# Kernel tuning notes

Measured on AMD Instinct MI355X. Metric: run time of the kernel, lower is better.

The kernel has to match this reference:

```python
import jax, jax.numpy as jnp
import numpy as np

DIM = 2048        # config.dim
HID = 1408        # config.moe_inter_dim
E = 16            # config.n_routed_experts
TOPK = 4          # config.n_activated_experts
SHARED = 2816     # n_shared_experts * moe_inter_dim
B, S = 1, 2048
ROUTE_SCALE = 1.0


def setup_inputs() -> dict:
    key = jax.random.key(0)
    ks = jax.random.split(key, 8)
    def w(k, shape, fan_in):
        return jax.random.normal(k, shape, jnp.float32) * (1.0 / np.sqrt(fan_in))
    return {
        "x": jax.random.normal(ks[0], (B, S, DIM), jnp.float32),
        "gate_w": w(ks[1], (E, DIM), DIM),
        "w1": w(ks[2], (E, HID, DIM), DIM),   # per-expert nn.Linear(dim, hid).weight
        "w2": w(ks[3], (E, DIM, HID), HID),   # per-expert nn.Linear(hid, dim).weight
        "w3": w(ks[4], (E, HID, DIM), DIM),
        "sw1": w(ks[5], (SHARED, DIM), DIM),  # shared MLP weights
        "sw2": w(ks[6], (DIM, SHARED), SHARED),
        "sw3": w(ks[7], (SHARED, DIM), DIM),
    }


def reference(x, gate_w, w1, w2, w3, sw1, sw2, sw3):
    shape = x.shape
    xt = x.reshape(-1, DIM)                      # [T, D]
    T = xt.shape[0]

    # --- Gate (score_func='softmax', n_groups=1, bias=None since dim != 7168) ---
    logits = xt @ gate_w.T                        # [T, E]
    scores = jax.nn.softmax(logits.astype(jnp.float32), axis=-1)
    topv, idx = jax.lax.top_k(scores, TOPK)       # n_groups==1: topk over flat scores
    weights = topv * ROUTE_SCALE                  # gather(original_scores, idx) == topv here

    # aux load-balance loss
    tpe = jnp.zeros((E,), jnp.float32).at[idx.reshape(-1)].add(1.0) / (T * TOPK)
    aux_loss = E * jnp.sum(tpe * scores.mean(axis=0))

    # --- Routed experts: combine weights [T, E], then batched SwiGLU GEMMs ---
    comb = jnp.zeros((T, E), jnp.float32).at[jnp.arange(T)[:, None], idx].add(weights)
    h = jax.nn.silu(jnp.einsum('td,ehd->teh', xt, w1)) * jnp.einsum('td,ehd->teh', xt, w3)
    y = jnp.einsum('teh,edh,te->td', h, w2, comb)  # weighted combine (0-weight experts cancel)

    # --- Shared experts (SwiGLU MLP, dropout=0) ---
    z = (jax.nn.silu(xt @ sw1.T) * (xt @ sw3.T)) @ sw2.T

    return (y + z).reshape(shape), aux_loss
```

## Files before the change

### kernel.cpp

```cpp
#include <hip/hip_runtime.h>
#include <hip/hip_bf16.h>

typedef unsigned short u16;
typedef __attribute__((ext_vector_type(8))) short short8;
typedef __attribute__((ext_vector_type(4))) float f32x4;

#define DIM 2048
#define HID 1408
#define NE 16
#define NTOK 2048
#define TOPK_ 4
#define SHID 2816
#define CAPROWS 10240
#define MAXTILES (CAPROWS / 128)
#define AUX_IDX (2048 * 2048)

__device__ inline u16 f2bf(float f) {
  __bf16 h = (__bf16)f;
  return __builtin_bit_cast(u16, h);
}

__device__ inline void gload_lds16(const void* g, void* l) {
  __builtin_amdgcn_global_load_lds(
      (const __attribute__((address_space(1))) unsigned int*)g,
      (__attribute__((address_space(3))) unsigned int*)l, 16, 0, 0);
}

__global__ __launch_bounds__(256) void gate_dots_kernel(
    const float* __restrict__ x, const float* __restrict__ gw,
    double* __restrict__ logits) {
  int t = blockIdx.x;
  const float* xt = x + (size_t)t * DIM;
  __shared__ double red[NE][4];
  int lane = threadIdx.x & 63, wid = threadIdx.x >> 6;
  for (int e = 0; e < NE; ++e) {
    const float* w = gw + e * DIM;
    double p = 0.0;
    for (int d = threadIdx.x; d < DIM; d += 256)
      p += (double)xt[d] * (double)w[d];
#pragma unroll
    for (int s = 32; s; s >>= 1) p += __shfl_xor(p, s);
    if (lane == 0) red[e][wid] = p;
  }
  __syncthreads();
  if (threadIdx.x < NE) {
    int e = threadIdx.x;
    logits[(size_t)t * NE + e] = red[e][0] + red[e][1] + red[e][2] + red[e][3];
  }
}

__global__ __launch_bounds__(256) void topk_kernel(
    const double* __restrict__ logits,
    int* __restrict__ idxb, float* __restrict__ wtb,
    int* __restrict__ counts, float* __restrict__ ssum) {
  __shared__ int lcnt[NE];
  __shared__ float lsum[NE];
  if (threadIdx.x < NE) { lcnt[threadIdx.x] = 0; lsum[threadIdx.x] = 0.f; }
  __syncthreads();
  int t = blockIdx.x * 256 + threadIdx.x;
  int lane = threadIdx.x & 63;
  double sc[NE];
  double m = -1e300;
#pragma unroll
  for (int e = 0; e < NE; ++e) {
    sc[e] = logits[(size_t)t * NE + e];
    if (sc[e] > m) m = sc[e];
  }
  double s = 0.0;
#pragma unroll
  for (int e = 0; e < NE; ++e) { sc[e] = exp(sc[e] - m); s += sc[e]; }
  double inv = 1.0 / s;
#pragma unroll
  for (int e = 0; e < NE; ++e) sc[e] *= inv;
  unsigned used = 0;
  for (int k = 0; k < TOPK_; ++k) {
    int be = 0; double bv = -1.0;
#pragma unroll
    for (int e = 0; e < NE; ++e)
      if (!((used >> e) & 1u) && sc[e] > bv) { bv = sc[e]; be = e; }
    used |= 1u << be;
    idxb[t * TOPK_ + k] = be;
    wtb[t * TOPK_ + k] = (float)bv;
    atomicAdd(&lcnt[be], 1);
  }
#pragma unroll
  for (int e = 0; e < NE; ++e) {
    float v = (float)sc[e];
#pragma unroll
    for (int sft = 32; sft; sft >>= 1) v += __shfl_xor(v, sft);
    if (lane == 0) atomicAdd(&lsum[e], v);
  }
  __syncthreads();
  if (threadIdx.x < NE) {
    atomicAdd(&counts[threadIdx.x], lcnt[threadIdx.x]);
    atomicAdd(&ssum[threadIdx.x], lsum[threadIdx.x]);
  }
}

__global__ __launch_bounds__(256) void setup_kernel(
    const int* __restrict__ counts, int* __restrict__ off, int* __restrict__ cap,
    const float* __restrict__ ssum, int* __restrict__ perm, float* __restrict__ pwt,
    float* __restrict__ aux_out,
    int* __restrict__ tile2e, int* __restrict__ tile2m0) {
  for (int i = threadIdx.x; i < MAXTILES; i += 256) tile2e[i] = -1;
  __syncthreads();
  if (threadIdx.x == 0) {
    int o = 0; double aux = 0.0; int nt = 0;
    for (int e = 0; e < NE; ++e) {
      off[e] = o;
      int c = (counts[e] + 127) & ~127;
      cap[e] = c;
      for (int t = 0; t < (c >> 7); ++t) {
        int slot = (nt / 10) + (nt % 10) * 8;
        tile2e[slot] = e;
        tile2m0[slot] = o + t * 128;
        ++nt;
      }
      o += c;
      aux += ((double)counts[e] / (NTOK * TOPK_)) * ((double)ssum[e] / NTOK);
    }
    aux_out[0] = (float)(NE * aux);
  }
  for (int i = threadIdx.x; i < CAPROWS; i += 256) { perm[i] = 0; pwt[i] = 0.f; }
}

__global__ __launch_bounds__(256) void scatter_kernel(
    const int* __restrict__ idxb, const float* __restrict__ wtb,
    const int* __restrict__ off, int* __restrict__ cursor,
    int* __restrict__ perm, float* __restrict__ pwt) {
  int t = blockIdx.x * 256 + threadIdx.x;
  if (t >= NTOK) return;
  for (int k = 0; k < TOPK_; ++k) {
    int e = idxb[t * TOPK_ + k];
    int s = atomicAdd(&cursor[e], 1);
    int p = off[e] + s;
    perm[p] = t;
    pwt[p] = wtb[t * TOPK_ + k];
  }
}

__global__ __launch_bounds__(256) void cvtN_kernel(const float* __restrict__ in,
                                                   u16* __restrict__ out, long n) {
  long stride = (long)gridDim.x * 2048;
  for (long i = ((long)blockIdx.x * 256 + threadIdx.x) * 8; i < n; i += stride) {
    float4 a = *(const float4*)(in + i);
    float4 b = *(const float4*)(in + i + 4);
    union { u16 u[8]; uint4 v; } o;
    o.u[0] = f2bf(a.x); o.u[1] = f2bf(a.y); o.u[2] = f2bf(a.z); o.u[3] = f2bf(a.w);
    o.u[4] = f2bf(b.x); o.u[5] = f2bf(b.y); o.u[6] = f2bf(b.z); o.u[7] = f2bf(b.w);
    *(uint4*)(out + i) = o.v;
  }
}

template <bool GATHER, bool DUAL, int EPI>
__global__ __launch_bounds__(256) void gemm5_kernel(
    const u16* __restrict__ A, int lda,
    const float* __restrict__ B1, const float* __restrict__ B3,
    int ldb, long bstride, int K,
    const int* __restrict__ tile2e, const int* __restrict__ tile2m0,
    const int* __restrict__ seg_off, const int* __restrict__ seg_cnt,
    const int* __restrict__ perm, const float* __restrict__ pwt,
    float* __restrict__ C0, int ldc0,
    u16* __restrict__ Cb, int ldcb, int Mfixed) {
  int e, m0, rowlim;
  if (tile2e) {
    e = tile2e[blockIdx.x];
    if (e < 0) return;
    m0 = tile2m0[blockIdx.x];
    rowlim = seg_off[e] + seg_cnt[e];
  } else {
    e = 0;
    m0 = blockIdx.x * 128;
    if (m0 >= Mfixed) return;
    rowlim = Mfixed;
  }
  int n0 = blockIdx.y * 64;
  const float* Bb1 = B1 + (long)e * bstride;
  const float* Bb3 = DUAL ? (B3 + (long)e * bstride) : nullptr;

  __shared__ u16 As[128 * 64];
  __shared__ u16 Bs1[64 * 64];
  __shared__ u16 Bs3[DUAL ? 64 * 64 : 1];

  int tid = threadIdx.x;
  int lane = tid & 63;
  int wid = tid >> 6;
  int wr = wid >> 1, wc = wid & 1;

  f32x4 acc1[4][2], acc3[4][2];
#pragma unroll
  for (int mi = 0; mi < 4; ++mi)
#pragma unroll
    for (int ni = 0; ni < 2; ++ni) {
      acc1[mi][ni] = (f32x4){0.f, 0.f, 0.f, 0.f};
      acc3[mi][ni] = (f32x4){0.f, 0.f, 0.f, 0.f};
    }

  int ar = tid >> 3;
  int ac = (tid & 7) * 8;
  long abase[4];
#pragma unroll
  for (int it = 0; it < 4; ++it) {
    int row = m0 + it * 32 + ar;
    int rid = GATHER ? perm[row] : row;
    abase[it] = (long)rid * lda + ac;
  }
  int brr = tid >> 4;
  int bsl = (tid & 15) * 4;
  long bbase[4];
#pragma unroll
  for (int it = 0; it < 4; ++it)
    bbase[it] = (long)(n0 + it * 16 + brr) * ldb + bsl;

  float4 r1[4], r3[4];

  auto stageA = [&](int k0) {
#pragma unroll
    for (int it = 0; it < 4; ++it)
      gload_lds16(A + abase[it] + k0, &As[(it * 32 + ar) * 64 + ac]);
  };
  auto loadB = [&](int k0) {
#pragma unroll
    for (int it = 0; it < 4; ++it) r1[it] = *(const float4*)(Bb1 + bbase[it] + k0);
    if (DUAL) {
#pragma unroll
      for (int it = 0; it < 4; ++it) r3[it] = *(const float4*)(Bb3 + bbase[it] + k0);
    }
  };
  auto writeB = [&]() {
#pragma unroll
    for (int it = 0; it < 4; ++it) {
      int lo = (it * 16 + brr) * 64 + bsl;
      ushort4 o;
      o.x = f2bf(r1[it].x); o.y = f2bf(r1[it].y); o.z = f2bf(r1[it].z); o.w = f2bf(r1[it].w);
      *(ushort4*)&Bs1[lo] = o;
      if (DUAL) {
        ushort4 q;
        q.x = f2bf(r3[it].x); q.y = f2bf(r3[it].y); q.z = f2bf(r3[it].z); q.w = f2bf(r3[it].w);
        *(ushort4*)&Bs3[lo] = q;
      }
    }
  };

  loadB(0);
  int NT = K >> 6;
  for (int t = 0; t < NT; ++t) {
    if (t) __syncthreads();
    stageA(t << 6);
    writeB();
    __syncthreads();
    if (t + 1 < NT) loadB((t + 1) << 6);
#pragma unroll
    for (int kk = 0; kk < 64; kk += 32) {
      short8 af[4], b1f[2], b3f[2];
#pragma unroll
      for (int i = 0; i < 4; ++i)
        af[i] = *(const short8*)&As[(wr * 64 + i * 16 + (lane & 15)) * 64 + kk + (lane >> 4) * 8];
#pragma unroll
      for (int i = 0; i < 2; ++i)
        b1f[i] = *(const short8*)&Bs1[(wc * 32 + i * 16 + (lane & 15)) * 64 + kk + (lane >> 4) * 8];
      if (DUAL) {
#pragma unroll
        for (int i = 0; i < 2; ++i)
          b3f[i] = *(const short8*)&Bs3[(wc * 32 + i * 16 + (lane & 15)) * 64 + kk + (lane >> 4) * 8];
      }
#pragma unroll
      for (int mi = 0; mi < 4; ++mi)
#pragma unroll
        for (int ni = 0; ni < 2; ++ni) {
          acc1[mi][ni] = __builtin_amdgcn_mfma_f32_16x16x32_bf16(af[mi], b1f[ni], acc1[mi][ni], 0, 0, 0);
          if (DUAL)
            acc3[mi][ni] = __builtin_amdgcn_mfma_f32_16x16x32_bf16(af[mi], b3f[ni], acc3[mi][ni], 0, 0, 0);
        }
    }
  }

  int rbase = m0 + wr * 64 + (lane >> 4) * 4;
  int cbase = n0 + wc * 32 + (lane & 15);
#pragma unroll
  for (int mi = 0; mi < 4; ++mi) {
#pragma unroll
    for (int ni = 0; ni < 2; ++ni) {
      int col = cbase + ni * 16;
#pragma unroll
      for (int r = 0; r < 4; ++r) {
        int row = rbase + mi * 16 + r;
        float v = acc1[mi][ni][r];
        if (EPI == 0) {
          float a3 = acc3[mi][ni][r];
          float sg = v / (1.f + __expf(-v));
          Cb[(long)row * ldcb + col] = f2bf(sg * a3);
        } else if (EPI == 1) {
          C0[(long)row * ldc0 + col] = v;
        } else {
          if (row < rowlim) {
            atomicAdd(&C0[(long)perm[row] * ldc0 + col], v * pwt[row]);
          }
        }
      }
    }
  }
}

extern "C" void kernel_launch(void* const* d_in, const int* in_sizes, int n_in,
                              void* d_out, int out_size, void* d_ws, size_t ws_size,
                              hipStream_t stream) {
  (void)in_sizes; (void)n_in; (void)out_size; (void)ws_size;
  const float* x   = (const float*)d_in[0];
  const float* gw  = (const float*)d_in[1];
  const float* w1  = (const float*)d_in[2];
  const float* w2  = (const float*)d_in[3];
  const float* w3  = (const float*)d_in[4];
  const float* sw1 = (const float*)d_in[5];
  const float* sw2 = (const float*)d_in[6];
  const float* sw3 = (const float*)d_in[7];
  float* out = (float*)d_out;
  char* ws = (char*)d_ws;

  int*   counts = (int*)(ws + 0);
  int*   cursor = (int*)(ws + 64);
  int*   off    = (int*)(ws + 128);
  int*   cap    = (int*)(ws + 192);
  float* ssum   = (float*)(ws + 256);
  int*   tile2e = (int*)(ws + 1024);
  int*   tile2m0= (int*)(ws + 2048);
  int*   idxb   = (int*)(ws + 4096);
  float* wtb    = (float*)(ws + 4096 + 32768);
  int*   perm   = (int*)(ws + 4096 + 65536);
  float* pwt    = (float*)(ws + 4096 + 65536 + 40960);
  u16*   xb     = (u16*)(ws + 262144);
  double* logits = (double*)(ws + 8650752);
  u16*   hbuf   = (u16*)(ws + 16777216);
  u16*   hsb    = (u16*)(ws + 45613056);

  hipMemsetAsync(ws, 0, 512, stream);
  gate_dots_kernel<<<dim3(NTOK), dim3(256), 0, stream>>>(x, gw, logits);
  topk_kernel<<<dim3(NTOK / 256), dim3(256), 0, stream>>>(logits, idxb, wtb, counts, ssum);
  setup_kernel<<<dim3(1), dim3(256), 0, stream>>>(counts, off, cap, ssum, perm, pwt,
                                                  out + AUX_IDX, tile2e, tile2m0);
  scatter_kernel<<<dim3(8), dim3(256), 0, stream>>>(idxb, wtb, off, cursor, perm, pwt);
  cvtN_kernel<<<dim3(2048), dim3(256), 0, stream>>>(x, xb, (long)NTOK * DIM);

  gemm5_kernel<true, true, 0><<<dim3(MAXTILES, HID / 64, 1), dim3(256), 0, stream>>>(
      xb, DIM, w1, w3, DIM, (long)HID * DIM, DIM, tile2e, tile2m0,
      off, counts, perm, pwt, nullptr, 0, hbuf, HID, 0);
  gemm5_kernel<false, true, 0><<<dim3(NTOK / 128, SHID / 64, 1), dim3(256), 0, stream>>>(
      xb, DIM, sw1, sw3, DIM, 0, DIM, nullptr, nullptr,
      nullptr, nullptr, nullptr, nullptr, nullptr, 0, hsb, SHID, NTOK);
  gemm5_kernel<false, false, 1><<<dim3(NTOK / 128, DIM / 64, 1), dim3(256), 0, stream>>>(
      hsb, SHID, sw2, nullptr, SHID, 0, SHID, nullptr, nullptr,
      nullptr, nullptr, nullptr, nullptr, out, DIM, nullptr, 0, NTOK);
  gemm5_kernel<false, false, 2><<<dim3(MAXTILES, DIM / 64, 1), dim3(256), 0, stream>>>(
      hbuf, HID, w2, nullptr, HID, (long)DIM * HID, HID, tile2e, tile2m0,
      off, counts, perm, pwt, out, DIM, nullptr, 0, 0);
}
```

Baseline: 706.6 us.

## Stage fp32 weights into LDS via direct global-to-LDS loads with XOR swizzle

Weight tiles now go straight from global memory into shared memory as fp32 using async global-to-LDS loads, instead of passing through registers and being converted to bf16 before the LDS write. The bf16 conversion moves to fragment-read time. Both A and B tiles get an XOR-swizzled layout to avoid LDS bank conflicts. The register-level prefetch of the next B tile is dropped, leaving a simple load, sync, compute, sync loop. In exchange, the fp32 B tiles double LDS use (up to 48KB with dual weights), which can cut occupancy, and the conversion is repeated in every wave that reads the same B fragment.

```diff
diff --git a/kernel.cpp b/kernel.cpp
--- a/kernel.cpp
+++ b/kernel.cpp
@@ -153,7 +153,7 @@
 }
 
 template <bool GATHER, bool DUAL, int EPI>
-__global__ __launch_bounds__(256) void gemm5_kernel(
+__global__ __launch_bounds__(256) void gemm6_kernel(
     const u16* __restrict__ A, int lda,
     const float* __restrict__ B1, const float* __restrict__ B3,
     int ldb, long bstride, int K,
@@ -179,8 +179,8 @@
   const float* Bb3 = DUAL ? (B3 + (long)e * bstride) : nullptr;
 
   __shared__ u16 As[128 * 64];
-  __shared__ u16 Bs1[64 * 64];
-  __shared__ u16 Bs3[DUAL ? 64 * 64 : 1];
+  __shared__ float Bs1[64 * 64];
+  __shared__ float Bs3[DUAL ? 64 * 64 : 1];
 
   int tid = threadIdx.x;
   int lane = tid & 63;
@@ -196,73 +196,68 @@
       acc3[mi][ni] = (f32x4){0.f, 0.f, 0.f, 0.f};
     }
 
-  int ar = tid >> 3;
-  int ac = (tid & 7) * 8;
+  int sr = tid >> 3;
+  int scA = tid & 7;
   long abase[4];
 #pragma unroll
   for (int it = 0; it < 4; ++it) {
-    int row = m0 + it * 32 + ar;
+    int row = m0 + it * 32 + sr;
     int rid = GATHER ? perm[row] : row;
-    abase[it] = (long)rid * lda + ac;
-  }
-  int brr = tid >> 4;
-  int bsl = (tid & 15) * 4;
+    abase[it] = (long)rid * lda + ((scA ^ (sr & 7)) << 3);
+  }
+  int br = tid >> 4;
+  int scB = tid & 15;
   long bbase[4];
 #pragma unroll
   for (int it = 0; it < 4; ++it)
-    bbase[it] = (long)(n0 + it * 16 + brr) * ldb + bsl;
-
-  float4 r1[4], r3[4];
-
-  auto stageA = [&](int k0) {
+    bbase[it] = (long)(n0 + it * 16 + br) * ldb + ((scB ^ (br & 7)) << 2);
+
+  for (int k0 = 0; k0 < K; k0 += 64) {
 #pragma unroll
     for (int it = 0; it < 4; ++it)
-      gload_lds16(A + abase[it] + k0, &As[(it * 32 + ar) * 64 + ac]);
-  };
-  auto loadB = [&](int k0) {
-#pragma unroll
-    for (int it = 0; it < 4; ++it) r1[it] = *(const float4*)(Bb1 + bbase[it] + k0);
+      gload_lds16(A + abase[it] + k0, &As[(it * 32 + sr) * 64 + scA * 8]);
+#pragma unroll
+    for (int it = 0; it < 4; ++it)
+      gload_lds16(Bb1 + bbase[it] + k0, &Bs1[(it * 16 + br) * 64 + scB * 4]);
     if (DUAL) {
 #pragma unroll
-      for (int it = 0; it < 4; ++it) r3[it] = *(const float4*)(Bb3 + bbase[it] + k0);
-    }
-  };
-  auto writeB = [&]() {
-#pragma unroll
-    for (int it = 0; it < 4; ++it) {
-      int lo = (it * 16 + brr) * 64 + bsl;
-      ushort4 o;
-      o.x = f2bf(r1[it].x); o.y = f2bf(r1[it].y); o.z = f2bf(r1[it].z); o.w = f2bf(r1[it].w);
-      *(ushort4*)&Bs1[lo] = o;
-      if (DUAL) {
-        ushort4 q;
-        q.x = f2bf(r3[it].x); q.y = f2bf(r3[it].y); q.z = f2bf(r3[it].z); q.w = f2bf(r3[it].w);
-        *(ushort4*)&Bs3[lo] = q;
+      for (int it = 0; it < 4; ++it)
+        gload_lds16(Bb3 + bbase[it] + k0, &Bs3[(it * 16 + br) * 64 + scB * 4]);
+    }
+    __syncthreads();
+#pragma unroll
+    for (int kk = 0; kk < 64; kk += 32) {
+      short8 af[4];
+#pragma unroll
+      for (int i = 0; i < 4; ++i) {
+        int R = wr * 64 + i * 16 + (lane & 15);
+        int c = (kk >> 3) + (lane >> 4);
+        af[i] = *(const short8*)&As[R * 64 + ((c ^ (R & 7)) << 3)];
       }
-    }
-  };
-
-  loadB(0);
-  int NT = K >> 6;
-  for (int t = 0; t < NT; ++t) {
-    if (t) __syncthreads();
-    stageA(t << 6);
-    writeB();
-    __syncthreads();
-    if (t + 1 < NT) loadB((t + 1) << 6);
-#pragma unroll
-    for (int kk = 0; kk < 64; kk += 32) {
-      short8 af[4], b1f[2], b3f[2];
-#pragma unroll
-      for (int i = 0; i < 4; ++i)
-        af[i] = *(const short8*)&As[(wr * 64 + i * 16 + (lane & 15)) * 64 + kk + (lane >> 4) * 8];
-#pragma unroll
-      for (int i = 0; i < 2; ++i)
-        b1f[i] = *(const short8*)&Bs1[(wc * 32 + i * 16 + (lane & 15)) * 64 + kk + (lane >> 4) * 8];
-      if (DUAL) {
-#pragma unroll
-        for (int i = 0; i < 2; ++i)
-          b3f[i] = *(const short8*)&Bs3[(wc * 32 + i * 16 + (lane & 15)) * 64 + kk + (lane >> 4) * 8];
+      short8 b1f[2], b3f[2];
+#pragma unroll
+      for (int i = 0; i < 2; ++i) {
+        int r = wc * 32 + i * 16 + (lane & 15);
+        int cB = (kk >> 2) + ((lane >> 4) << 1);
+        int s7 = r & 7;
+        f32x4 lo = *(const f32x4*)&Bs1[r * 64 + ((cB ^ s7) << 2)];
+        f32x4 hi = *(const f32x4*)&Bs1[r * 64 + (((cB + 1) ^ s7) << 2)];
+        short8 f;
+        f[0] = (short)f2bf(lo[0]); f[1] = (short)f2bf(lo[1]);
+        f[2] = (short)f2bf(lo[2]); f[3] = (short)f2bf(lo[3]);
+        f[4] = (short)f2bf(hi[0]); f[5] = (short)f2bf(hi[1]);
+        f[6] = (short)f2bf(hi[2]); f[7] = (short)f2bf(hi[3]);
+        b1f[i] = f;
+        if (DUAL) {
+          f32x4 lo3 = *(const f32x4*)&Bs3[r * 64 + ((cB ^ s7) << 2)];
+          f32x4 hi3 = *(const f32x4*)&Bs3[r * 64 + (((cB + 1) ^ s7) << 2)];
+          short8 g;
+          g[0] = (short)f2bf(lo3[0]); g[1] = (short)f2bf(lo3[1]);
+          g[2] = (short)f2bf(lo3[2]); g[3] = (short)f2bf(lo3[3]);
+          g[4] = (short)f2bf(hi3[0]); g[5] = (short)f2bf(hi3[1]);
+          g[6] = (short)f2bf(hi3[2]); g[7] = (short)f2bf(hi3[3]);
+          b3f[i] = g;
+        }
       }
 #pragma unroll
       for (int mi = 0; mi < 4; ++mi)
@@ -273,6 +268,7 @@
             acc3[mi][ni] = __builtin_amdgcn_mfma_f32_16x16x32_bf16(af[mi], b3f[ni], acc3[mi][ni], 0, 0, 0);
         }
     }
+    __syncthreads();
   }
 
   int rbase = m0 + wr * 64 + (lane >> 4) * 4;
@@ -341,16 +337,16 @@
   scatter_kernel<<<dim3(8), dim3(256), 0, stream>>>(idxb, wtb, off, cursor, perm, pwt);
   cvtN_kernel<<<dim3(2048), dim3(256), 0, stream>>>(x, xb, (long)NTOK * DIM);
 
-  gemm5_kernel<true, true, 0><<<dim3(MAXTILES, HID / 64, 1), dim3(256), 0, stream>>>(
+  gemm6_kernel<true, true, 0><<<dim3(MAXTILES, HID / 64), dim3(256), 0, stream>>>(
       xb, DIM, w1, w3, DIM, (long)HID * DIM, DIM, tile2e, tile2m0,
       off, counts, perm, pwt, nullptr, 0, hbuf, HID, 0);
-  gemm5_kernel<false, true, 0><<<dim3(NTOK / 128, SHID / 64, 1), dim3(256), 0, stream>>>(
+  gemm6_kernel<false, true, 0><<<dim3(NTOK / 128, SHID / 64), dim3(256), 0, stream>>>(
       xb, DIM, sw1, sw3, DIM, 0, DIM, nullptr, nullptr,
       nullptr, nullptr, nullptr, nullptr, nullptr, 0, hsb, SHID, NTOK);
-  gemm5_kernel<false, false, 1><<<dim3(NTOK / 128, DIM / 64, 1), dim3(256), 0, stream>>>(
+  gemm6_kernel<false, false, 1><<<dim3(NTOK / 128, DIM / 64), dim3(256), 0, stream>>>(
       hsb, SHID, sw2, nullptr, SHID, 0, SHID, nullptr, nullptr,
       nullptr, nullptr, nullptr, nullptr, out, DIM, nullptr, 0, NTOK);
-  gemm5_kernel<false, false, 2><<<dim3(MAXTILES, DIM / 64, 1), dim3(256), 0, stream>>>(
+  gemm6_kernel<false, false, 2><<<dim3(MAXTILES, DIM / 64), dim3(256), 0, stream>>>(
       hbuf, HID, w2, nullptr, HID, (long)DIM * HID, HID, tile2e, tile2m0,
       off, counts, perm, pwt, out, DIM, nullptr, 0, 0);
 }
```

Result: faster. 654.5 us (-7.4%).

## Double-buffer GEMM LDS tiles and XOR-swizzle LDS layout to avoid bank conflicts

Applied to the files above, without the earlier changes.

Converts the bf16 MFMA GEMM main loop to double-buffered LDS. The next A tile is issued through global_load_lds and the next B tile is prefetched into registers while the current tile is computed, with explicit vmcnt waits and barriers. It also XOR-swizzles the 16-byte column chunks of the A and B LDS tiles to cut bank conflicts on the short8 fragment reads. The cost is twice the LDS footprint, which may lower occupancy, and the hand-written waitcnt counts, which must match the exact number of outstanding loads.

```diff
diff --git a/kernel.cpp b/kernel.cpp
--- a/kernel.cpp
+++ b/kernel.cpp
@@ -153,7 +153,7 @@
 }
 
 template <bool GATHER, bool DUAL, int EPI>
-__global__ __launch_bounds__(256) void gemm5_kernel(
+__global__ __launch_bounds__(256) void gemm7_kernel(
     const u16* __restrict__ A, int lda,
     const float* __restrict__ B1, const float* __restrict__ B3,
     int ldb, long bstride, int K,
@@ -178,9 +178,9 @@
   const float* Bb1 = B1 + (long)e * bstride;
   const float* Bb3 = DUAL ? (B3 + (long)e * bstride) : nullptr;
 
-  __shared__ u16 As[128 * 64];
-  __shared__ u16 Bs1[64 * 64];
-  __shared__ u16 Bs3[DUAL ? 64 * 64 : 1];
+  __shared__ u16 As[2][128 * 64];
+  __shared__ u16 Bs1[2][64 * 64];
+  __shared__ u16 Bs3[DUAL ? 2 : 1][DUAL ? 64 * 64 : 1];
 
   int tid = threadIdx.x;
   int lane = tid & 63;
@@ -196,28 +196,29 @@
       acc3[mi][ni] = (f32x4){0.f, 0.f, 0.f, 0.f};
     }
 
-  int ar = tid >> 3;
-  int ac = (tid & 7) * 8;
+  int sr = tid >> 3;
+  int scA = tid & 7;
   long abase[4];
 #pragma unroll
   for (int it = 0; it < 4; ++it) {
-    int row = m0 + it * 32 + ar;
+    int row = m0 + it * 32 + sr;
     int rid = GATHER ? perm[row] : row;
-    abase[it] = (long)rid * lda + ac;
+    abase[it] = (long)rid * lda + ((scA ^ (sr & 7)) << 3);
   }
   int brr = tid >> 4;
-  int bsl = (tid & 15) * 4;
+  int gB = tid & 15;
+  int wofs = (((gB >> 1) ^ (brr & 7)) << 3) + ((gB & 1) << 2);
   long bbase[4];
 #pragma unroll
   for (int it = 0; it < 4; ++it)
-    bbase[it] = (long)(n0 + it * 16 + brr) * ldb + bsl;
+    bbase[it] = (long)(n0 + it * 16 + brr) * ldb + gB * 4;
 
   float4 r1[4], r3[4];
 
-  auto stageA = [&](int k0) {
+  auto stageA = [&](int buf, int k0) {
 #pragma unroll
     for (int it = 0; it < 4; ++it)
-      gload_lds16(A + abase[it] + k0, &As[(it * 32 + ar) * 64 + ac]);
+      gload_lds16(A + abase[it] + k0, &As[buf][(it * 32 + sr) * 64 + scA * 8]);
   };
   auto loadB = [&](int k0) {
 #pragma unroll
@@ -227,42 +228,56 @@
       for (int it = 0; it < 4; ++it) r3[it] = *(const float4*)(Bb3 + bbase[it] + k0);
     }
   };
-  auto writeB = [&]() {
+  auto writeB = [&](int buf) {
 #pragma unroll
     for (int it = 0; it < 4; ++it) {
-      int lo = (it * 16 + brr) * 64 + bsl;
+      int lo = (it * 16 + brr) * 64 + wofs;
       ushort4 o;
       o.x = f2bf(r1[it].x); o.y = f2bf(r1[it].y); o.z = f2bf(r1[it].z); o.w = f2bf(r1[it].w);
-      *(ushort4*)&Bs1[lo] = o;
+      *(ushort4*)&Bs1[buf][lo] = o;
       if (DUAL) {
         ushort4 q;
         q.x = f2bf(r3[it].x); q.y = f2bf(r3[it].y); q.z = f2bf(r3[it].z); q.w = f2bf(r3[it].w);
-        *(ushort4*)&Bs3[lo] = q;
+        *(ushort4*)&Bs3[buf][lo] = q;
       }
     }
   };
 
   loadB(0);
+  stageA(0, 0);
   int NT = K >> 6;
+  int cur = 0;
   for (int t = 0; t < NT; ++t) {
-    if (t) __syncthreads();
-    stageA(t << 6);
-    writeB();
-    __syncthreads();
-    if (t + 1 < NT) loadB((t + 1) << 6);
+    int nxt = cur ^ 1;
+    writeB(cur);
+    if (t + 1 < NT) {
+      loadB((t + 1) << 6);
+      stageA(nxt, (t + 1) << 6);
+      if (DUAL) asm volatile("s_waitcnt vmcnt(12)" ::: "memory");
+      else      asm volatile("s_waitcnt vmcnt(8)"  ::: "memory");
+    } else {
+      asm volatile("s_waitcnt vmcnt(0)" ::: "memory");
+    }
+    asm volatile("s_waitcnt lgkmcnt(0)" ::: "memory");
+    __builtin_amdgcn_sched_barrier(0);
+    __builtin_amdgcn_s_barrier();
+    __builtin_amdgcn_sched_barrier(0);
 #pragma unroll
     for (int kk = 0; kk < 64; kk += 32) {
       short8 af[4], b1f[2], b3f[2];
 #pragma unroll
-      for (int i = 0; i < 4; ++i)
-        af[i] = *(const short8*)&As[(wr * 64 + i * 16 + (lane & 15)) * 64 + kk + (lane >> 4) * 8];
-#pragma unroll
-      for (int i = 0; i < 2; ++i)
-        b1f[i] = *(const short8*)&Bs1[(wc * 32 + i * 16 + (lane & 15)) * 64 + kk + (lane >> 4) * 8];
-      if (DUAL) {
-#pragma unroll
-        for (int i = 0; i < 2; ++i)
-          b3f[i] = *(const short8*)&Bs3[(wc * 32 + i * 16 + (lane & 15)) * 64 + kk + (lane >> 4) * 8];
+      for (int i = 0; i < 4; ++i) {
+        int R = wr * 64 + i * 16 + (lane & 15);
+        int c = (kk >> 3) + (lane >> 4);
+        af[i] = *(const short8*)&As[cur][R * 64 + ((c ^ (R & 7)) << 3)];
+      }
+#pragma unroll
+      for (int i = 0; i < 2; ++i) {
+        int r = wc * 32 + i * 16 + (lane & 15);
+        int cR = (kk >> 3) + (lane >> 4);
+        b1f[i] = *(const short8*)&Bs1[cur][r * 64 + ((cR ^ (r & 7)) << 3)];
+        if (DUAL)
+          b3f[i] = *(const short8*)&Bs3[cur][r * 64 + ((cR ^ (r & 7)) << 3)];
       }
 #pragma unroll
       for (int mi = 0; mi < 4; ++mi)
@@ -273,6 +288,9 @@
             acc3[mi][ni] = __builtin_amdgcn_mfma_f32_16x16x32_bf16(af[mi], b3f[ni], acc3[mi][ni], 0, 0, 0);
         }
     }
+    __builtin_amdgcn_sched_barrier(0);
+    __builtin_amdgcn_s_barrier();
+    cur = nxt;
   }
 
   int rbase = m0 + wr * 64 + (lane >> 4) * 4;
@@ -341,16 +359,16 @@
   scatter_kernel<<<dim3(8), dim3(256), 0, stream>>>(idxb, wtb, off, cursor, perm, pwt);
   cvtN_kernel<<<dim3(2048), dim3(256), 0, stream>>>(x, xb, (long)NTOK * DIM);
 
-  gemm5_kernel<true, true, 0><<<dim3(MAXTILES, HID / 64, 1), dim3(256), 0, stream>>>(
+  gemm7_kernel<true, true, 0><<<dim3(MAXTILES, HID / 64), dim3(256), 0, stream>>>(
       xb, DIM, w1, w3, DIM, (long)HID * DIM, DIM, tile2e, tile2m0,
       off, counts, perm, pwt, nullptr, 0, hbuf, HID, 0);
-  gemm5_kernel<false, true, 0><<<dim3(NTOK / 128, SHID / 64, 1), dim3(256), 0, stream>>>(
+  gemm7_kernel<false, true, 0><<<dim3(NTOK / 128, SHID / 64), dim3(256), 0, stream>>>(
       xb, DIM, sw1, sw3, DIM, 0, DIM, nullptr, nullptr,
       nullptr, nullptr, nullptr, nullptr, nullptr, 0, hsb, SHID, NTOK);
-  gemm5_kernel<false, false, 1><<<dim3(NTOK / 128, DIM / 64, 1), dim3(256), 0, stream>>>(
+  gemm7_kernel<false, false, 1><<<dim3(NTOK / 128, DIM / 64), dim3(256), 0, stream>>>(
       hsb, SHID, sw2, nullptr, SHID, 0, SHID, nullptr, nullptr,
       nullptr, nullptr, nullptr, nullptr, out, DIM, nullptr, 0, NTOK);
-  gemm5_kernel<false, false, 2><<<dim3(MAXTILES, DIM / 64, 1), dim3(256), 0, stream>>>(
+  gemm7_kernel<false, false, 2><<<dim3(MAXTILES, DIM / 64), dim3(256), 0, stream>>>(
       hbuf, HID, w2, nullptr, HID, (long)DIM * HID, HID, tile2e, tile2m0,
       off, counts, perm, pwt, out, DIM, nullptr, 0, 0);
 }
```

Result: faster. 642.7 us (-9.0%).
